# Optimization experiments

Hardware: AMD Instinct MI355X
Metric: run time of the kernel (lower is better)

## Reference

```python
import jax, jax.numpy as jnp
import numpy as np

GAMMA = 1.0        # soft-min temperature for differentiable DTW
BIG = 1e9          # value for cells outside the Sakoe-Chiba band
DTW_BW = 0.2       # band width as fraction of normalized path deviation
AVG_T_LEN = True   # divide discrepancy by input sequence length


def _softmin3(a, b, c):
    # differentiable min over the three DP predecessors
    z = jnp.stack([a, b, c], axis=0)
    return -GAMMA * jax.nn.logsumexp(-z / GAMMA, axis=0)


def _dtw(C, mask):
    """Band-limited soft-DTW DP. C: [T,K] pairwise costs, mask: [T,K] bool band.
    Returns scalar D[T-1,K-1]. Row scan over T; inner scan over K carries the
    left neighbor (recurrence D[i,j] = C[i,j] + softmin(D[i-1,j], D[i,j-1], D[i-1,j-1]))."""
    T, K = C.shape

    def row_step(carry, inp):
        prev_row, diag0 = carry            # prev_row: D[i-1,:]; diag0: virtual D[i-1,-1]
        c_row, m_row = inp
        diag = jnp.concatenate([diag0[None], prev_row[:-1]])  # D[i-1,j-1]

        def col_step(left, xs):
            c, up, dg, m = xs
            d = c + _softmin3(up, left, dg)
            d = jnp.where(m, d, BIG)       # kill cells outside the band
            return d, d

        _, row = jax.lax.scan(col_step, jnp.float32(BIG), (c_row, prev_row, diag, m_row))
        return (row, jnp.float32(BIG)), None

    # virtual border: D[-1,-1] = 0, all other border cells = BIG
    init = (jnp.full((K,), BIG, dtype=jnp.float32), jnp.float32(0.0))
    (last_row, _), _ = jax.lax.scan(row_step, init, (C, mask))
    return last_row[-1]


def setup_inputs() -> dict:
    key = jax.random.key(0)
    kx, kp = jax.random.split(key)
    B, T = 64, 512
    F, K = 32, 64
    x = jax.random.normal(kx, (B, T), dtype=jnp.float32)
    protos = jax.random.normal(kp, (F, K), dtype=jnp.float32)  # learnable DTW kernels
    return {"x": x, "protos": protos}


def reference(x, protos):
    B, T = x.shape
    F, K = protos.shape
    # pairwise squared costs: [B, F, T, K]
    C = (x[:, None, :, None] - protos[None, :, None, :]) ** 2
    # Sakoe-Chiba band on normalized coordinates
    ii = jnp.arange(T, dtype=jnp.float32) / (T - 1)
    jj = jnp.arange(K, dtype=jnp.float32) / (K - 1)
    mask = jnp.abs(ii[:, None] - jj[None, :]) <= DTW_BW  # [T, K]
    d = jax.vmap(jax.vmap(lambda c: _dtw(c, mask)))(C)    # [B, F]
    if AVG_T_LEN:
        d = d / jnp.float32(T)
    return d[:, :, None]  # [B, num_filter, out_len=1]
```

## Files before the change

### kernel.cpp

```cpp
#include <hip/hip_runtime.h>

#define T_LEN  512
#define K_LEN  64
#define NFILT  32
#define NBATCH 64
#define XOFS   64
#define XS_SZ  (XOFS + 576)
#define NCHUNK 35
#define CHUNK  16
#define TAIL   15
#define SQRT_LOG2E 1.2011224087864498f
#define LN2        0.6931471805599453f

static __device__ __forceinline__ float wave_shr1(float x) {
    int r = __builtin_amdgcn_update_dpp(0, __builtin_bit_cast(int, x),
                                        0x138, 0xF, 0xF, true);
    return __builtin_bit_cast(float, r);
}

template <int N>
static __device__ __forceinline__ float row_ror(float x) {
    int r = __builtin_amdgcn_update_dpp(0, __builtin_bit_cast(int, x),
                                        0x120 + N, 0xF, 0xF, true);
    return __builtin_bit_cast(float, r);
}

static __device__ __forceinline__ float exp2_fast(float x) {
#if __has_builtin(__builtin_amdgcn_exp2f)
    return __builtin_amdgcn_exp2f(x);
#else
    return exp2f(x);
#endif
}

__global__ __launch_bounds__(256) void dtw_kernel(const float* __restrict__ x,
                                                  const float* __restrict__ protos,
                                                  float* __restrict__ out) {
    __shared__ float xs[XS_SZ];
    const int tid  = threadIdx.x;
    const int lane = tid & 63;
    const int wid  = tid >> 6;
    const int b    = blockIdx.x >> 3;
    const int f    = ((blockIdx.x & 7) << 2) | wid;

    for (int t = tid; t < XS_SZ; t += 256) {
        int i = t - XOFS;
        xs[t] = (i >= 0 && i < T_LEN) ? x[b * T_LEN + i] * SQRT_LOG2E : 0.0f;
    }
    __syncthreads();

    const float p  = protos[f * K_LEN + lane] * SQRT_LOG2E;
    const float jj = (float)lane / 63.0f;

    int a0 = 0, b0 = T_LEN - 1;
    while (a0 < b0) { int m = (a0 + b0) >> 1;
        if ((float)m / 511.0f - jj >= -0.2f) b0 = m; else a0 = m + 1; }
    const int ilo = a0;
    a0 = 0; b0 = T_LEN - 1;
    while (a0 < b0) { int m = (a0 + b0 + 1) >> 1;
        if ((float)m / 511.0f - jj <= 0.2f) a0 = m; else b0 = m - 1; }
    const int ihi = a0;

    const unsigned range = (unsigned)(ihi - ilo);
    unsigned t = (unsigned)(-(lane + ilo));
    float prev = 0.0f;
    float dgp  = (lane == 0) ? 1.0f : 0.0f;
    int   S2   = 0;
    int   xb   = XOFS - lane;

    for (int c = 0; c < NCHUNK; ++c) {
#pragma unroll
        for (int k = 0; k < CHUNK; ++k) {
            float xv   = xs[xb + k];
            float df   = xv - p;
            float w    = exp2_fast(-(df * df));
            w          = (t <= range) ? w : 0.0f;
            float left = wave_shr1(prev);
            float sum  = (prev + left) + dgp;
            dgp  = left;
            prev = sum * w;
            ++t;
        }
        xb += CHUNK;

        float m = prev;
        m = fmaxf(m, row_ror<8>(m));
        m = fmaxf(m, row_ror<4>(m));
        m = fmaxf(m, row_ror<2>(m));
        m = fmaxf(m, row_ror<1>(m));
        int mi = __builtin_bit_cast(int, m);
        unsigned m0 = (unsigned)__builtin_amdgcn_readlane(mi, 0);
        unsigned m1 = (unsigned)__builtin_amdgcn_readlane(mi, 16);
        unsigned m2 = (unsigned)__builtin_amdgcn_readlane(mi, 32);
        unsigned m3 = (unsigned)__builtin_amdgcn_readlane(mi, 48);
        unsigned ma = m0 > m1 ? m0 : m1;
        unsigned mb = m2 > m3 ? m2 : m3;
        unsigned mx = ma > mb ? ma : mb;
        int e  = (int)((mx >> 23) & 0xFF);
        int Me = 284 - e;
        Me = Me < 1 ? 1 : (Me > 254 ? 254 : Me);
        float M = __builtin_bit_cast(float, Me << 23);
        S2  += Me - 127;
        prev *= M;
        dgp  *= M;
    }
#pragma unroll
    for (int k = 0; k < TAIL; ++k) {
        float xv   = xs[xb + k];
        float df   = xv - p;
        float w    = exp2_fast(-(df * df));
        w          = (t <= range) ? w : 0.0f;
        float left = wave_shr1(prev);
        float sum  = (prev + left) + dgp;
        dgp  = left;
        prev = sum * w;
        ++t;
    }

    if (lane == 63) {
        float D = ((float)S2 - log2f(prev)) * LN2;
        out[b * NFILT + f] = D * (1.0f / (float)T_LEN);
    }
}

extern "C" void kernel_launch(void* const* d_in, const int* in_sizes, int n_in,
                              void* d_out, int out_size, void* d_ws, size_t ws_size,
                              hipStream_t stream) {
    const float* x      = (const float*)d_in[0];
    const float* protos = (const float*)d_in[1];
    float* out          = (float*)d_out;

    dim3 grid(NBATCH * (NFILT / 4));
    dim3 block(256);
    hipLaunchKernelGGL(dtw_kernel, grid, block, 0, stream, x, protos, out);
}
```

Measured before the change: 33.21 us.

## Double-buffer LDS reads into registers and reassociate wavefront DP step

The anti-diagonal wavefront loop now prefetches the next 32 x values from LDS into a register buffer while the current buffer is consumed, so LDS latency is taken off the serial DP chain. The chunk size grows from 16 to 32, which halves how often the cross-lane max renormalization runs. The step is reassociated so prev+dgp is computed before the DPP shift result arrives, shortening the dependent chain. The cost is higher register pressure from the 64 buffered values, and renormalizing less often carries some risk of float overflow or underflow over 32 steps.

After: 31.14 us. -6.2%, faster.

```diff
diff --git a/kernel.cpp b/kernel.cpp
--- a/kernel.cpp
+++ b/kernel.cpp
@@ -5,10 +5,8 @@
 #define NFILT  32
 #define NBATCH 64
 #define XOFS   64
-#define XS_SZ  (XOFS + 576)
-#define NCHUNK 35
-#define CHUNK  16
-#define TAIL   15
+#define XS_SZ  640
+#define CHUNK  32
 #define SQRT_LOG2E 1.2011224087864498f
 #define LN2        0.6931471805599453f
 
@@ -43,9 +41,9 @@
     const int b    = blockIdx.x >> 3;
     const int f    = ((blockIdx.x & 7) << 2) | wid;
 
-    for (int t = tid; t < XS_SZ; t += 256) {
-        int i = t - XOFS;
-        xs[t] = (i >= 0 && i < T_LEN) ? x[b * T_LEN + i] * SQRT_LOG2E : 0.0f;
+    for (int t0 = tid; t0 < XS_SZ; t0 += 256) {
+        int i = t0 - XOFS;
+        xs[t0] = (i >= 0 && i < T_LEN) ? x[b * T_LEN + i] * SQRT_LOG2E : 0.0f;
     }
     __syncthreads();
 
@@ -66,61 +64,75 @@
     float prev = 0.0f;
     float dgp  = (lane == 0) ? 1.0f : 0.0f;
     int   S2   = 0;
-    int   xb   = XOFS - lane;
+    int   base = XOFS - lane;
 
-    for (int c = 0; c < NCHUNK; ++c) {
+    float A[CHUNK], B[CHUNK];
 #pragma unroll
-        for (int k = 0; k < CHUNK; ++k) {
-            float xv   = xs[xb + k];
-            float df   = xv - p;
-            float w    = exp2_fast(-(df * df));
-            w          = (t <= range) ? w : 0.0f;
-            float left = wave_shr1(prev);
-            float sum  = (prev + left) + dgp;
-            dgp  = left;
-            prev = sum * w;
-            ++t;
-        }
-        xb += CHUNK;
+    for (int k = 0; k < CHUNK; ++k) A[k] = xs[base + k];
 
-        float m = prev;
-        m = fmaxf(m, row_ror<8>(m));
-        m = fmaxf(m, row_ror<4>(m));
-        m = fmaxf(m, row_ror<2>(m));
-        m = fmaxf(m, row_ror<1>(m));
-        int mi = __builtin_bit_cast(int, m);
-        unsigned m0 = (unsigned)__builtin_amdgcn_readlane(mi, 0);
-        unsigned m1 = (unsigned)__builtin_amdgcn_readlane(mi, 16);
-        unsigned m2 = (unsigned)__builtin_amdgcn_readlane(mi, 32);
-        unsigned m3 = (unsigned)__builtin_amdgcn_readlane(mi, 48);
-        unsigned ma = m0 > m1 ? m0 : m1;
-        unsigned mb = m2 > m3 ? m2 : m3;
-        unsigned mx = ma > mb ? ma : mb;
-        int e  = (int)((mx >> 23) & 0xFF);
-        int Me = 284 - e;
-        Me = Me < 1 ? 1 : (Me > 254 ? 254 : Me);
-        float M = __builtin_bit_cast(float, Me << 23);
-        S2  += Me - 127;
-        prev *= M;
-        dgp  *= M;
+#define STEP(XV) do {                                   \
+        float df_   = (XV) - p;                         \
+        float w_    = exp2_fast(-(df_ * df_));          \
+        w_          = (t <= range) ? w_ : 0.0f;         \
+        float a_    = prev + dgp;        \
+        float left_ = wave_shr1(prev);                  \
+        dgp  = left_;                                   \
+        prev = (a_ + left_) * w_;                       \
+        ++t;                                            \
+    } while (0)
+
+#define RENORM() do {                                                        \
+        float m_ = prev;                                                     \
+        m_ = fmaxf(m_, row_ror<8>(m_));                                      \
+        m_ = fmaxf(m_, row_ror<4>(m_));                                      \
+        m_ = fmaxf(m_, row_ror<2>(m_));                                      \
+        m_ = fmaxf(m_, row_ror<1>(m_));                                      \
+        int mi_ = __builtin_bit_cast(int, m_);                               \
+        unsigned r0_ = (unsigned)__builtin_amdgcn_readlane(mi_, 0);          \
+        unsigned r1_ = (unsigned)__builtin_amdgcn_readlane(mi_, 16);         \
+        unsigned r2_ = (unsigned)__builtin_amdgcn_readlane(mi_, 32);         \
+        unsigned r3_ = (unsigned)__builtin_amdgcn_readlane(mi_, 48);         \
+        unsigned ra_ = r0_ > r1_ ? r0_ : r1_;                                \
+        unsigned rb_ = r2_ > r3_ ? r2_ : r3_;                                \
+        unsigned mx_ = ra_ > rb_ ? ra_ : rb_;                                \
+        int e_  = (int)((mx_ >> 23) & 0xFF);                                 \
+        int Me_ = 284 - e_;                                                  \
+        Me_ = Me_ < 1 ? 1 : (Me_ > 254 ? 254 : Me_);                         \
+        float M_ = __builtin_bit_cast(float, Me_ << 23);                     \
+        S2  += Me_ - 127;                                                    \
+        prev *= M_;                                                          \
+        dgp  *= M_;                                                          \
+    } while (0)
+
+#pragma unroll 1
+    for (int cc = 0; cc < 8; ++cc) {
+#pragma unroll
+        for (int k = 0; k < CHUNK; ++k) B[k] = xs[base + CHUNK + k];
+#pragma unroll
+        for (int k = 0; k < CHUNK; ++k) STEP(A[k]);
+        RENORM();
+        base += CHUNK;
+#pragma unroll
+        for (int k = 0; k < CHUNK; ++k) A[k] = xs[base + CHUNK + k];
+#pragma unroll
+        for (int k = 0; k < CHUNK; ++k) STEP(B[k]);
+        RENORM();
+        base += CHUNK;
     }
 #pragma unroll
-    for (int k = 0; k < TAIL; ++k) {
-        float xv   = xs[xb + k];
-        float df   = xv - p;
-        float w    = exp2_fast(-(df * df));
-        w          = (t <= range) ? w : 0.0f;
-        float left = wave_shr1(prev);
-        float sum  = (prev + left) + dgp;
-        dgp  = left;
-        prev = sum * w;
-        ++t;
-    }
+    for (int k = 0; k < CHUNK; ++k) B[k] = xs[base + CHUNK + k];
+#pragma unroll
+    for (int k = 0; k < CHUNK; ++k) STEP(A[k]);
+    RENORM();
+#pragma unroll
+    for (int k = 0; k < 31; ++k) STEP(B[k]);
 
     if (lane == 63) {
         float D = ((float)S2 - log2f(prev)) * LN2;
         out[b * NFILT + f] = D * (1.0f / (float)T_LEN);
     }
+#undef STEP
+#undef RENORM
 }
 
 extern "C" void kernel_launch(void* const* d_in, const int* in_sizes, int n_in,
```
